# Optimization experiments

Measured on AMD Instinct MI355X. Metric: run time of the kernel, lower is better.

The kernel has to match this reference:

```python
import jax, jax.numpy as jnp
import numpy as np

FEAT_STRIDE = 8
SCALES = (4.0, 8.0, 16.0)
RATIOS = (0.5, 1.0, 2.0)
A = len(SCALES) * len(RATIOS)          # 9 anchors per location
PRE_NMS = 2048
POST_NMS = 300
NMS_THRESH = 0.7


def _gen_base_anchors():
    # cube anchors at scale*stride, ratio applied to depth; boxes (x1,y1,z1,x2,y2,z2)
    base = float(FEAT_STRIDE)
    ctr = (base - 1.0) / 2.0
    boxes = []
    for r in RATIOS:
        for s in SCALES:
            w = h = base * s
            d = base * s * r
            boxes.append([ctr - 0.5 * (w - 1), ctr - 0.5 * (h - 1), ctr - 0.5 * (d - 1),
                          ctr + 0.5 * (w - 1), ctr + 0.5 * (h - 1), ctr + 0.5 * (d - 1)])
    return jnp.asarray(boxes, jnp.float32)  # [A,6]


def _all_anchors(D, H, W):
    sz = jnp.arange(D, dtype=jnp.float32) * FEAT_STRIDE
    sy = jnp.arange(H, dtype=jnp.float32) * FEAT_STRIDE
    sx = jnp.arange(W, dtype=jnp.float32) * FEAT_STRIDE
    zz, yy, xx = jnp.meshgrid(sz, sy, sx, indexing='ij')  # order (d,h,w) matches score layout
    shifts = jnp.stack([xx, yy, zz, xx, yy, zz], -1).reshape(-1, 6)  # [K,6]
    return (shifts[:, None, :] + _gen_base_anchors()[None]).reshape(-1, 6)  # [K*A,6]


def _apply_deltas(anchors, deltas):
    w = anchors[:, 3] - anchors[:, 0] + 1.0
    h = anchors[:, 4] - anchors[:, 1] + 1.0
    d = anchors[:, 5] - anchors[:, 2] + 1.0
    cx = anchors[:, 0] + 0.5 * w
    cy = anchors[:, 1] + 0.5 * h
    cz = anchors[:, 2] + 0.5 * d
    dx, dy, dz, dw, dh, dd = [deltas[:, i] for i in range(6)]
    pcx = dx * w + cx; pcy = dy * h + cy; pcz = dz * d + cz
    pw = jnp.exp(dw) * w; ph = jnp.exp(dh) * h; pd = jnp.exp(dd) * d
    return jnp.stack([pcx - 0.5 * pw, pcy - 0.5 * ph, pcz - 0.5 * pd,
                      pcx + 0.5 * pw, pcy + 0.5 * ph, pcz + 0.5 * pd], -1)


def _clip_boxes(boxes, iminfo):  # iminfo = [D_im, H_im, W_im]
    lo = jnp.zeros((6,), boxes.dtype)
    hi = jnp.stack([iminfo[2], iminfo[1], iminfo[0], iminfo[2], iminfo[1], iminfo[0]]) - 1.0
    return jnp.clip(boxes, lo[None, :], hi[None, :])


def _pairwise_iou3d(b):  # b: [N,6]
    lo = jnp.maximum(b[:, None, :3], b[None, :, :3])          # [N,N,3]
    hi = jnp.minimum(b[:, None, 3:], b[None, :, 3:])
    inter = jnp.prod(jnp.clip(hi - lo + 1.0, 0.0), axis=-1)   # [N,N]
    vol = jnp.prod(b[:, 3:] - b[:, :3] + 1.0, axis=-1)        # [N]
    return inter / (vol[:, None] + vol[None, :] - inter)


def _nms_keep(iou):
    N = iou.shape[0]
    idx = jnp.arange(N)
    def body(i, keep):
        sup = (iou[i] > NMS_THRESH) & keep[i] & (idx > i)
        return keep & ~sup
    return jax.lax.fori_loop(0, N, body, jnp.ones((N,), bool))


def _propose_one(scores, deltas, anchors, iminfo):
    boxes = _clip_boxes(_apply_deltas(anchors, deltas), iminfo)  # [KA,6]
    _, order = jax.lax.top_k(scores, PRE_NMS)
    b = boxes[order]                                             # [PRE,6], score-sorted desc
    keep = _nms_keep(_pairwise_iou3d(b))
    key = jnp.where(keep, jnp.arange(PRE_NMS), PRE_NMS)
    sel = jnp.argsort(key)[:POST_NMS]                            # first POST_NMS kept, in score order
    valid = (key[sel] < PRE_NMS).astype(b.dtype)
    return b[sel] * valid[:, None]                               # zero-padded rows if < POST_NMS kept


def _forward(base_feat, im_info, W_conv, b_conv, W_cls, b_cls, W_bbox, b_bbox):
    B, C, D, H, W = base_feat.shape
    x = jax.lax.conv_general_dilated(
        base_feat, W_conv, (1, 1, 1), ((1, 1), (1, 1), (1, 1)),
        dimension_numbers=('NCDHW', 'OIDHW', 'NCDHW'))
    x = jax.nn.relu(x + b_conv[None, :, None, None, None])       # [B,512,D,H,W]
    cls = jnp.einsum('bcdhw,oc->bodhw', x, W_cls) + b_cls[None, :, None, None, None]
    prob = jax.nn.softmax(cls.reshape(B, 2, A, D, H, W), axis=1)  # reshape(x,2) + softmax(dim=1)
    fg = prob[:, 1]                                               # [B,A,D,H,W]
    scores = jnp.transpose(fg, (0, 2, 3, 4, 1)).reshape(B, -1)    # [B, K*A], order (d,h,w,a)
    bb = jnp.einsum('bcdhw,oc->bodhw', x, W_bbox) + b_bbox[None, :, None, None, None]
    deltas = jnp.transpose(bb.reshape(B, A, 6, D, H, W), (0, 3, 4, 5, 1, 2)).reshape(B, -1, 6)
    anchors = _all_anchors(D, H, W)
    rois6 = jax.vmap(lambda s, d, im: _propose_one(s, d, anchors, im))(scores, deltas, im_info)
    bidx = jnp.broadcast_to(jnp.arange(B, dtype=rois6.dtype)[:, None, None], (B, POST_NMS, 1))
    return jnp.concatenate([bidx, rois6], -1)                     # [B, POST_NMS, 7]


def setup_inputs() -> dict:
    key = jax.random.key(0)
    ks = jax.random.split(key, 4)
    B, din, D, H, W = 2, 128, 8, 32, 32
    base_feat = jax.random.normal(ks[0], (B, din, D, H, W), jnp.float32)
    im_info = jnp.asarray([[64.0, 256.0, 256.0]] * B, jnp.float32)  # (D_im, H_im, W_im)
    gt_boxes = jnp.zeros((B, 20, 7), jnp.float32)
    num_boxes = jnp.zeros((B,), jnp.int64)
    W_conv = jax.random.normal(ks[1], (512, din, 3, 3, 3), jnp.float32) * 0.02
    b_conv = jnp.zeros((512,), jnp.float32)
    W_cls = jax.random.normal(ks[2], (2 * A, 512), jnp.float32) * 0.01
    b_cls = jnp.zeros((2 * A,), jnp.float32)
    W_bbox = jax.random.normal(ks[3], (6 * A, 512), jnp.float32) * 0.01
    b_bbox = jnp.zeros((6 * A,), jnp.float32)
    return {"base_feat": base_feat, "im_info": im_info, "gt_boxes": gt_boxes,
            "num_boxes": num_boxes, "W_conv": W_conv, "b_conv": b_conv,
            "W_cls": W_cls, "b_cls": b_cls, "W_bbox": W_bbox, "b_bbox": b_bbox}


def reference(base_feat, im_info, gt_boxes, num_boxes, W_conv, b_conv, W_cls, b_cls, W_bbox, b_bbox):
    # Eval-mode RPN forward: losses are 0 in the original; gt_boxes/num_boxes unused.
    rois = _forward(base_feat, im_info, W_conv, b_conv, W_cls, b_cls, W_bbox, b_bbox)
    return rois
```

## Files before the change

kernel.cpp:

```cpp
#include <hip/hip_runtime.h>
#include <stdint.h>

#define BATCH 2
#define CIN 128
#define COUT 512
#define DD 8
#define PSPAT 8192
#define NA 9
#define NANCH 73728
#define PRE 2048
#define POST 300
#define CAP 4096
#define NMS_TH 0.7f

typedef unsigned short u16;
typedef _Float16 f16x8 __attribute__((ext_vector_type(8)));
typedef float f32x16 __attribute__((ext_vector_type(16)));
typedef unsigned int uint32x4 __attribute__((ext_vector_type(4)));

constexpr size_t OFF_WT   = 0;
constexpr size_t OFF_WHT  = 7077888;
constexpr size_t OFF_X    = 7241728;
constexpr size_t OFF_SC   = 40796160;
constexpr size_t OFF_BX   = 41385984;
constexpr size_t OFF_SB   = 44957696;
constexpr size_t OFF_MK   = 45056000;
constexpr size_t OFF_HIST = 16;
constexpr size_t OFF_CAND = 524304;
constexpr size_t OFF_XH   = 46104576;
constexpr size_t OFF_XL   = 50298880;
constexpr size_t WS_NEED_FAST = 54493184;

#define NT_WT   (27 * 128 * 512)
#define NT_WHT  (512 * 80)
__global__ void k_wtrans(const float* __restrict__ Wc, u16* __restrict__ Wg,
                         const float* __restrict__ Wcls, const float* __restrict__ Wbb,
                         float* __restrict__ Wht) {
    int e = blockIdx.x * blockDim.x + threadIdx.x;
    if (e < NT_WT) {
        const int k    = e & 63;
        const int n    = (e >> 6) & 127;
        const int half = (e >> 13) & 1;
        const int rest = e >> 14;
        const int co = (rest / 27) * 128 + n;
        const int ci = half * 64 + k;
        const int tp = rest % 27;
        const float v = Wc[(co * 128 + ci) * 27 + tp] * 1024.f;
        const _Float16 h = (_Float16)v;
        const _Float16 l = (_Float16)(v - (float)h);
        char* rb = (char*)Wg + (((size_t)(rest * 2 + half)) << 15) + n * 256;
        const int hcol = (k >> 3) ^ (n & 15);
        const int lcol = ((k >> 3) | 8) ^ (n & 15);
        const int kb = (k & 7) << 1;
        *(u16*)(rb + (hcol << 4) + kb) = __builtin_bit_cast(unsigned short, h);
        *(u16*)(rb + (lcol << 4) + kb) = __builtin_bit_cast(unsigned short, l);
        return;
    }
    e -= NT_WT;
    if (e >= NT_WHT) return;
    int q = e % 80;
    int c = e / 80;
    int og = q / 10, k = q % 10;
    int o = og * 9 + k;
    float v = 0.f;
    if (k < 9) v = (o < 18) ? Wcls[o * 512 + c] : Wbb[(o - 18) * 512 + c];
    Wht[e] = v;
}

__global__ __launch_bounds__(256) void k_split(const float* __restrict__ in,
                                               u16* __restrict__ xh, u16* __restrict__ xl) {
    __shared__ float t[128][33];
    const int blk = blockIdx.x;
    const int b = blk >> 8, d = (blk >> 5) & 7, h = blk & 31;
    const int tid = threadIdx.x;
    const float* src = in + ((size_t)b << 20) + d * 1024 + h * 32;
    #pragma unroll
    for (int i = 0; i < 16; ++i) {
        const int e = tid + i * 256;
        const int ci = e >> 5, w = e & 31;
        t[ci][w] = src[(size_t)ci * 8192 + w];
    }
    __syncthreads();
    const size_t ob = (size_t)((b * 8 + d) * 32 + h) * 4096;
    #pragma unroll
    for (int i = 0; i < 2; ++i) {
        const int e = tid + i * 256;
        const int oct = e >> 5, w = e & 31;
        unsigned sh0, sh1, sh2, sh3, sl0, sl1, sl2, sl3;
        #define SPL2(C, SH, SL) { \
            const float va_ = t[oct * 8 + 2*(C)][w] * 1024.f; \
            const float vb_ = t[oct * 8 + 2*(C)+1][w] * 1024.f; \
            const _Float16 ha_ = (_Float16)va_, hb_ = (_Float16)vb_; \
            const _Float16 la_ = (_Float16)(va_ - (float)ha_); \
            const _Float16 lb_ = (_Float16)(vb_ - (float)hb_); \
            SH = (unsigned)__builtin_bit_cast(unsigned short, ha_) | \
                 ((unsigned)__builtin_bit_cast(unsigned short, hb_) << 16); \
            SL = (unsigned)__builtin_bit_cast(unsigned short, la_) | \
                 ((unsigned)__builtin_bit_cast(unsigned short, lb_) << 16); }
        SPL2(0, sh0, sl0) SPL2(1, sh1, sl1) SPL2(2, sh2, sl2) SPL2(3, sh3, sl3)
        #undef SPL2
        uint32x4 vh = {sh0, sh1, sh2, sh3};
        uint32x4 vl = {sl0, sl1, sl2, sl3};
        *(uint32x4*)(xh + ob + (size_t)e * 8) = vh;
        *(uint32x4*)(xl + ob + (size_t)e * 8) = vl;
    }
}

#define MFMA(A, B, C) __builtin_amdgcn_mfma_f32_32x32x16_f16((A), (B), (C), 0, 0, 0)
#define Z16 {0.f,0.f,0.f,0.f,0.f,0.f,0.f,0.f,0.f,0.f,0.f,0.f,0.f,0.f,0.f,0.f}

#define WISSUE(S, BUF) { \
    const int tap_ = t0 + ((S) >> 1); \
    const char* gw_ = WgB + (((size_t)((nt * 27 + tap_) * 2 + ((S) & 1))) << 15) \
                    + (wv << 13) + ln16; \
    char* lb_ = smem + ((BUF) << 15) + (wv << 13); \
    _Pragma("unroll") \
    for (int j_ = 0; j_ < 8; ++j_) \
        __builtin_amdgcn_global_load_lds( \
            (const __attribute__((address_space(1))) void*)(gw_ + (j_ << 10)), \
            (__attribute__((address_space(3))) void*)(lb_ + (j_ << 10)), 16, 0, 0); }

#define KKSTEP(KK, BH0, BL0, BH1, BL1) { \
    const int ch_ = ((((KK) << 1) + cq) ^ rsw) << 4; \
    const int cl_ = (((((KK) << 1) + cq) | 8) ^ rsw) << 4; \
    const char* r0_ = wb_ + (rm0 << 8); \
    const char* r1_ = wb_ + (rm1 << 8); \
    const f16x8 wh0 = *(const f16x8*)(r0_ + ch_); \
    const f16x8 wl0 = *(const f16x8*)(r0_ + cl_); \
    const f16x8 wh1 = *(const f16x8*)(r1_ + ch_); \
    const f16x8 wl1 = *(const f16x8*)(r1_ + cl_); \
    acc00 = MFMA(wh0, BH0, acc00); \
    acc01 = MFMA(wh0, BH1, acc01); \
    acc10 = MFMA(wh1, BH0, acc10); \
    acc11 = MFMA(wh1, BH1, acc11); \
    acc00 = MFMA(wh0, BL0, acc00); \
    acc01 = MFMA(wh0, BL1, acc01); \
    acc10 = MFMA(wh1, BL0, acc10); \
    acc11 = MFMA(wh1, BL1, acc11); \
    acc00 = MFMA(wl0, BH0, acc00); \
    acc01 = MFMA(wl0, BH1, acc01); \
    acc10 = MFMA(wl1, BH0, acc10); \
    acc11 = MFMA(wl1, BH1, acc11); }

#define EPI(ACC, MI, NI) { \
    const int coB_ = co0 + (wm << 6) + ((MI) << 5) + hl4; \
    const int pt_  = p0 + (wn << 6) + ((NI) << 5) + l31; \
    _Pragma("unroll") \
    for (int g_ = 0; g_ < 4; ++g_) { \
        _Pragma("unroll") \
        for (int q_ = 0; q_ < 4; ++q_) { \
            const int co_ = coB_ + (g_ << 3) + q_; \
            const float v_ = ACC[g_ * 4 + q_] * 9.5367431640625e-07f + bconv[co_]; \
            x[((size_t)((b << 9) + co_) << 13) + pt_] = fmaxf(v_, 0.f); \
        } } }

#define FLD(N, KK, BH, BL) { \
    const int h2_ = hb_ + (N); \
    const bool ok_ = okw_ && ((unsigned)h2_ < 32u); \
    const size_t ix_ = sbase_ + ((size_t)(h2_ & 31) << 12); \
    const f16x8 vh_ = *(const f16x8*)(xh + ix_ + ((KK) << 9)); \
    const f16x8 vl_ = *(const f16x8*)(xl + ix_ + ((KK) << 9)); \
    BH = ok_ ? vh_ : fz8; \
    BL = ok_ ? vl_ : fz8; }

#define ALOADF(S, P) { \
    const int tap_ = t0 + ((S) >> 1); \
    const int kd_ = tap_ / 9, kh_ = (tap_ / 3) % 3, kw_ = tap_ % 3; \
    const int id_ = d0 + kd_ - 1; \
    const int w2_ = l31 + kw_ - 1; \
    const bool okw_ = (unsigned)w2_ < 32u; \
    const int hb_ = h0 + (wn << 1) + kh_ - 1; \
    const int oc0_ = (((S) & 1) << 3) + cq; \
    const size_t sbase_ = (((size_t)((b << 3) + id_)) << 17) + (oc0_ << 8) + ((w2_ & 31) << 3); \
    FLD(0, 0, P##h00, P##l00) FLD(0, 1, P##h01, P##l01) \
    FLD(0, 2, P##h02, P##l02) FLD(0, 3, P##h03, P##l03) \
    FLD(1, 0, P##h10, P##l10) FLD(1, 1, P##h11, P##l11) \
    FLD(1, 2, P##h12, P##l12) FLD(1, 3, P##h13, P##l13) }

#define COMPUTEF(BUF, P) { \
    const char* wb_ = smem + ((BUF) << 15); \
    KKSTEP(0, P##h00, P##l00, P##h10, P##l10) \
    KKSTEP(1, P##h01, P##l01, P##h11, P##l11) \
    KKSTEP(2, P##h02, P##l02, P##h12, P##l12) \
    KKSTEP(3, P##h03, P##l03, P##h13, P##l13) }

#define VMCNT24 asm volatile("s_waitcnt vmcnt(24)" ::: "memory");
#define VMCNT16 asm volatile("s_waitcnt vmcnt(16)" ::: "memory");
#define VMCNT0  asm volatile("s_waitcnt vmcnt(0)"  ::: "memory");
#define SBAR    __builtin_amdgcn_s_barrier();
#define SCHED0  __builtin_amdgcn_sched_barrier(0);

__global__ __launch_bounds__(256, 2) void k_conv_f(const u16* __restrict__ xh,
                                                   const u16* __restrict__ xl,
                                                   const u16* __restrict__ Wg,
                                                   const float* __restrict__ bconv,
                                                   float* __restrict__ x) {
    __shared__ __align__(16) char smem[65536];
    const int tid  = threadIdx.x;
    const int bx   = blockIdx.x;
    const int nt   = blockIdx.y;
    const int b    = blockIdx.z;
    const int p0   = bx << 7;
    const int d0   = bx >> 3;
    const int h0   = (bx & 7) << 2;
    const int co0  = nt << 7;

    const int lane = tid & 63;
    const int wv   = tid >> 6;
    const int wm   = wv & 1;
    const int wn   = wv >> 1;
    const int l31  = lane & 31;
    const int cq   = lane >> 5;
    const int hl4  = cq << 2;
    const int rsw  = l31 & 15;
    const int rm0  = (wm << 6) + l31;
    const int rm1  = rm0 + 32;
    const int ln16 = lane << 4;

    const int t0   = (d0 == 0) ? 9 : 0;
    const int nTap = 27 - (((d0 == 0) || (d0 == 7)) ? 9 : 0);
    const int NS   = nTap * 2;

    const char* WgB = (const char*)Wg;
    const f16x8 fz8 = {(_Float16)0.f, (_Float16)0.f, (_Float16)0.f, (_Float16)0.f,
                       (_Float16)0.f, (_Float16)0.f, (_Float16)0.f, (_Float16)0.f};

    f16x8 Ah00, Al00, Ah01, Al01, Ah02, Al02, Ah03, Al03,
          Ah10, Al10, Ah11, Al11, Ah12, Al12, Ah13, Al13;
    f16x8 Bh00, Bl00, Bh01, Bl01, Bh02, Bl02, Bh03, Bl03,
          Bh10, Bl10, Bh11, Bl11, Bh12, Bl12, Bh13, Bl13;
    f32x16 acc00 = Z16, acc01 = Z16, acc10 = Z16, acc11 = Z16;

    WISSUE(0, 0)
    SCHED0
    ALOADF(0, A)
    VMCNT16
    SBAR

    for (int s = 0; s < NS; s += 2) {
        WISSUE(s + 1, 1)
        SCHED0
        ALOADF(s + 1, B)
        VMCNT24
        SCHED0
        COMPUTEF(0, A)
        VMCNT16
        SBAR
        if (s + 2 < NS) {
            WISSUE(s + 2, 0)
            SCHED0
            ALOADF(s + 2, A)
            VMCNT24
        } else {
            VMCNT0
        }
        SCHED0
        COMPUTEF(1, B)
        if (s + 2 < NS) {
            VMCNT16
            SBAR
        }
    }

    EPI(acc00, 0, 0)
    EPI(acc01, 0, 1)
    EPI(acc10, 1, 0)
    EPI(acc11, 1, 1)
}

#define PK2(YA, YB, UH, UL) { \
    const float sa_ = (YA) * 1024.f, sb_ = (YB) * 1024.f; \
    const _Float16 ha_ = (_Float16)sa_, hb_ = (_Float16)sb_; \
    const _Float16 la_ = (_Float16)(sa_ - (float)ha_); \
    const _Float16 lb_ = (_Float16)(sb_ - (float)hb_); \
    UH = (unsigned)__builtin_bit_cast(unsigned short, ha_) | \
         ((unsigned)__builtin_bit_cast(unsigned short, hb_) << 16); \
    UL = (unsigned)__builtin_bit_cast(unsigned short, la_) | \
         ((unsigned)__builtin_bit_cast(unsigned short, lb_) << 16); }

#define BLDI(N, KK) { \
    const int h2_ = hb_ + (N); \
    const bool ok_ = okw_ && ((unsigned)h2_ < 32u); \
    const float* ap_ = in + (((size_t)(cb0_ + ((KK) << 4))) << 13) + spo_ + (h2_ << 5); \
    y[N][KK][0] = ok_ ? ap_[0]     : 0.f; \
    y[N][KK][1] = ok_ ? ap_[8192]  : 0.f; \
    y[N][KK][2] = ok_ ? ap_[16384] : 0.f; \
    y[N][KK][3] = ok_ ? ap_[24576] : 0.f; \
    y[N][KK][4] = ok_ ? ap_[32768] : 0.f; \
    y[N][KK][5] = ok_ ? ap_[40960] : 0.f; \
    y[N][KK][6] = ok_ ? ap_[49152] : 0.f; \
    y[N][KK][7] = ok_ ? ap_[57344] : 0.f; }

#define ALOADISS(S) { \
    const int tap_ = t0 + ((S) >> 1); \
    const int kd_ = tap_ / 9, kh_ = (tap_ / 3) % 3, kw_ = tap_ % 3; \
    const int id_ = d0 + kd_ - 1; \
    const int w2_ = l31 + kw_ - 1; \
    const bool okw_ = (unsigned)w2_ < 32u; \
    const int hb_ = h0 + (wn << 1) + kh_ - 1; \
    const int cb0_ = b * CIN + (((S) & 1) << 6) + (cq << 3); \
    const long long spo_ = ((long long)id_ << 10) + w2_; \
    BLDI(0, 0) BLDI(0, 1) BLDI(0, 2) BLDI(0, 3) \
    BLDI(1, 0) BLDI(1, 1) BLDI(1, 2) BLDI(1, 3) }

#define CVTFRAG(N, KK, BH, BL) { \
    unsigned uh0_, uh1_, uh2_, uh3_, ul0_, ul1_, ul2_, ul3_; \
    PK2(y[N][KK][0], y[N][KK][1], uh0_, ul0_) \
    PK2(y[N][KK][2], y[N][KK][3], uh1_, ul1_) \
    PK2(y[N][KK][4], y[N][KK][5], uh2_, ul2_) \
    PK2(y[N][KK][6], y[N][KK][7], uh3_, ul3_) \
    { uint32x4 th_ = {uh0_, uh1_, uh2_, uh3_}; BH = __builtin_bit_cast(f16x8, th_); } \
    { uint32x4 tl_ = {ul0_, ul1_, ul2_, ul3_}; BL = __builtin_bit_cast(f16x8, tl_); } }

#define CVTALL() { \
    CVTFRAG(0, 0, bh00, bl00) CVTFRAG(0, 1, bh01, bl01) \
    CVTFRAG(0, 2, bh02, bl02) CVTFRAG(0, 3, bh03, bl03) \
    CVTFRAG(1, 0, bh10, bl10) CVTFRAG(1, 1, bh11, bl11) \
    CVTFRAG(1, 2, bh12, bl12) CVTFRAG(1, 3, bh13, bl13) }

#define COMPUTE(BUF) { \
    const char* wb_ = smem + ((BUF) << 15); \
    KKSTEP(0, bh00, bl00, bh10, bl10) \
    KKSTEP(1, bh01, bl01, bh11, bl11) \
    KKSTEP(2, bh02, bl02, bh12, bl12) \
    KKSTEP(3, bh03, bl03, bh13, bl13) }

__global__ __launch_bounds__(256, 2) void k_conv(const float* __restrict__ in,
                                                 const u16* __restrict__ Wg,
                                                 const float* __restrict__ bconv,
                                                 float* __restrict__ x) {
    __shared__ __align__(16) char smem[65536];
    const int tid  = threadIdx.x;
    const int bx   = blockIdx.x;
    const int nt   = blockIdx.y;
    const int b    = blockIdx.z;
    const int p0   = bx << 7;
    const int d0   = bx >> 3;
    const int h0   = (bx & 7) << 2;
    const int co0  = nt << 7;

    const int lane = tid & 63;
    const int wv   = tid >> 6;
    const int wm   = wv & 1;
    const int wn   = wv >> 1;
    const int l31  = lane & 31;
    const int cq   = lane >> 5;
    const int hl4  = cq << 2;
    const int rsw  = l31 & 15;
    const int rm0  = (wm << 6) + l31;
    const int rm1  = rm0 + 32;
    const int ln16 = lane << 4;

    const int t0   = (d0 == 0) ? 9 : 0;
    const int nTap = 27 - (((d0 == 0) || (d0 == 7)) ? 9 : 0);
    const int NS   = nTap * 2;

    const char* WgB = (const char*)Wg;

    float y[2][4][8];
    f16x8 bh00, bh01, bh02, bh03, bh10, bh11, bh12, bh13;
    f16x8 bl00, bl01, bl02, bl03, bl10, bl11, bl12, bl13;
    f32x16 acc00 = Z16, acc01 = Z16, acc10 = Z16, acc11 = Z16;

    WISSUE(0, 0)
    ALOADISS(0)
    __syncthreads();

    for (int s = 0; s < NS; ++s) {
        if (s + 1 < NS) { WISSUE(s + 1, (s + 1) & 1) }
        CVTALL()
        __builtin_amdgcn_sched_barrier(0);
        if (s + 1 < NS) { ALOADISS(s + 1) }
        __builtin_amdgcn_sched_barrier(0);
        COMPUTE(s & 1)
        __syncthreads();
    }

    EPI(acc00, 0, 0)
    EPI(acc01, 0, 1)
    EPI(acc10, 1, 0)
    EPI(acc11, 1, 1)
}

__global__ __launch_bounds__(256) void k_heads(const float* __restrict__ x,
                                               const float* __restrict__ Wht,
                                               const float* __restrict__ bcls,
                                               const float* __restrict__ bbb,
                                               const float* __restrict__ iminfo,
                                               float* __restrict__ scores,
                                               float* __restrict__ boxes,
                                               unsigned int* __restrict__ hist) {
    __shared__ __align__(16) float smx[4096];
    __shared__ __align__(16) float Whs[2560];
    __shared__ __align__(16) float ex[10240];
    const int tid = threadIdx.x;
    const int p0  = blockIdx.x * 128;
    const int b   = blockIdx.y;
    const int pl  = tid & 31;
    const int og  = tid >> 5;

    float acc[4][9] = {};

    for (int cc = 0; cc < 512; cc += 32) {
        __syncthreads();
        #pragma unroll
        for (int i = 0; i < 4; ++i) {
            int e4 = tid + i * 256;
            int ch = e4 >> 5;
            int pt4 = (e4 & 31) * 4;
            *(float4*)&smx[ch * 128 + pt4] =
                *(const float4*)&x[((size_t)(b * COUT + cc + ch) << 13) + p0 + pt4];
        }
        #pragma unroll
        for (int i = 0; i < 10; ++i) {
            int e = tid + i * 256;
            Whs[e] = Wht[cc * 80 + e];
        }
        __syncthreads();
        for (int kk = 0; kk < 32; ++kk) {
            float4 a4 = *(const float4*)&smx[kk * 128 + pl * 4];
            const float* wp = &Whs[kk * 80 + og * 10];
            float2 w0 = *(const float2*)(wp);
            float2 w1 = *(const float2*)(wp + 2);
            float2 w2 = *(const float2*)(wp + 4);
            float2 w3 = *(const float2*)(wp + 6);
            float  w8 = wp[8];
            float wv[9] = {w0.x, w0.y, w1.x, w1.y, w2.x, w2.y, w3.x, w3.y, w8};
            #pragma unroll
            for (int k = 0; k < 9; ++k) {
                float wk = wv[k];
                acc[0][k] += a4.x * wk;
                acc[1][k] += a4.y * wk;
                acc[2][k] += a4.z * wk;
                acc[3][k] += a4.w * wk;
            }
        }
    }

    __syncthreads();
    #pragma unroll
    for (int pi = 0; pi < 4; ++pi)
        #pragma unroll
        for (int k = 0; k < 9; ++k)
            ex[(pl * 4 + pi) * 80 + og * 10 + k] = acc[pi][k];
    __syncthreads();

    if (tid < 128) {
        const int p = p0 + tid;
        float v[72];
        #pragma unroll
        for (int og2 = 0; og2 < 8; ++og2)
            #pragma unroll
            for (int k = 0; k < 9; ++k)
                v[og2 * 9 + k] = ex[tid * 80 + og2 * 10 + k];

        const float im0 = iminfo[b * 3 + 0], im1 = iminfo[b * 3 + 1], im2 = iminfo[b * 3 + 2];
        const float hix = im2 - 1.f, hiy = im1 - 1.f, hiz = im0 - 1.f;
        const int d = p >> 10, h = (p >> 5) & 31, w = p & 31;
        const float sx = w * 8.f, sy = h * 8.f, sz = d * 8.f;

        #pragma unroll 1
        for (int a = 0; a < 9; ++a) {
            float c0 = v[a] + bcls[a];
            float c1 = v[9 + a] + bcls[9 + a];
            float m  = fmaxf(c0, c1);
            float e0 = expf(c0 - m), e1 = expf(c1 - m);
            float sc = e1 / (e0 + e1);
            scores[b * NANCH + p * 9 + a] = sc;
            atomicAdd(&hist[b * 65536 + (__float_as_uint(sc) >> 16)], 1u);

            float aw = (float)(32 << (a % 3));
            float ad = aw * 0.5f * (float)(1 << (a / 3));
            float ax1 = sx + 3.5f - 0.5f * (aw - 1.f);
            float ax2 = sx + 3.5f + 0.5f * (aw - 1.f);
            float ay1 = sy + 3.5f - 0.5f * (aw - 1.f);
            float ay2 = sy + 3.5f + 0.5f * (aw - 1.f);
            float az1 = sz + 3.5f - 0.5f * (ad - 1.f);
            float az2 = sz + 3.5f + 0.5f * (ad - 1.f);
            float ww_ = ax2 - ax1 + 1.f, hh_ = ay2 - ay1 + 1.f, dd_ = az2 - az1 + 1.f;
            float cx = ax1 + 0.5f * ww_, cy = ay1 + 0.5f * hh_, cz = az1 + 0.5f * dd_;

            const float* dv = &v[18 + a * 6];
            float dx = dv[0] + bbb[a * 6 + 0];
            float dy = dv[1] + bbb[a * 6 + 1];
            float dz = dv[2] + bbb[a * 6 + 2];
            float dw = dv[3] + bbb[a * 6 + 3];
            float dh = dv[4] + bbb[a * 6 + 4];
            float dd2 = dv[5] + bbb[a * 6 + 5];
            float pcx = dx * ww_ + cx, pcy = dy * hh_ + cy, pcz = dz * dd_ + cz;
            float pw = expf(dw) * ww_, ph = expf(dh) * hh_, pd = expf(dd2) * dd_;
            float x1 = fminf(fmaxf(pcx - 0.5f * pw, 0.f), hix);
            float y1 = fminf(fmaxf(pcy - 0.5f * ph, 0.f), hiy);
            float z1 = fminf(fmaxf(pcz - 0.5f * pd, 0.f), hiz);
            float x2 = fminf(fmaxf(pcx + 0.5f * pw, 0.f), hix);
            float y2 = fminf(fmaxf(pcy + 0.5f * ph, 0.f), hiy);
            float z2 = fminf(fmaxf(pcz + 0.5f * pd, 0.f), hiz);
            float* bp = &boxes[(size_t)(b * NANCH + p * 9 + a) * 6];
            bp[0] = x1; bp[1] = y1; bp[2] = z1; bp[3] = x2; bp[4] = y2; bp[5] = z2;
        }
    }
}

__global__ __launch_bounds__(1024) void k_cutcompact(const float* __restrict__ scores,
                                                     const unsigned int* __restrict__ hist,
                                                     unsigned long long* __restrict__ cand) {
    __shared__ unsigned int cs[1024], scan[1024];
    __shared__ unsigned int sh_cut, sh_pos;
    const int b = blockIdx.x, tid = threadIdx.x;
    const unsigned int* h = hist + b * 65536;
    unsigned int s = 0;
    for (int i = 0; i < 64; ++i) s += h[tid * 64 + i];
    cs[tid] = s; scan[tid] = s;
    if (tid == 0) sh_pos = 0;
    __syncthreads();
    for (int d = 1; d < 1024; d <<= 1) {
        unsigned int v = scan[tid];
        unsigned int add = (tid + d < 1024) ? scan[tid + d] : 0u;
        __syncthreads();
        scan[tid] = v + add;
        __syncthreads();
    }
    unsigned int above = (tid + 1 < 1024) ? scan[tid + 1] : 0u;
    if (above < PRE && above + cs[tid] >= PRE) {
        unsigned int cum = above;
        for (int x = tid * 64 + 63; x >= tid * 64; --x) {
            cum += h[x];
            if (cum >= PRE) { sh_cut = (unsigned int)x; break; }
        }
    }
    __syncthreads();
    const unsigned int cut = sh_cut;
    const float* sc = scores + b * NANCH;
    for (int i = tid; i < NANCH; i += 1024) {
        unsigned int u = __float_as_uint(sc[i]);
        if ((u >> 16) >= cut) {
            unsigned int pos = atomicAdd(&sh_pos, 1u);
            if (pos < CAP) cand[b * CAP + pos] = ((unsigned long long)(~u) << 32) | (unsigned)i;
        }
    }
    __syncthreads();
    const unsigned int cnt = (sh_pos < CAP) ? sh_pos : CAP;
    for (int i = (int)cnt + tid; i < CAP; i += 1024)
        cand[b * CAP + i] = ~0ull;
}

__global__ __launch_bounds__(1024) void k_sort2(const unsigned long long* __restrict__ cand,
                                                const float* __restrict__ boxes,
                                                float* __restrict__ sboxes) {
    __shared__ unsigned long long sk[CAP];
    const int b = blockIdx.x, tid = threadIdx.x;
    for (int i = tid; i < CAP; i += 1024) sk[i] = cand[b * CAP + i];
    __syncthreads();
    for (int k = 2; k <= CAP; k <<= 1) {
        for (int j = k >> 1; j > 0; j >>= 1) {
            #pragma unroll 1
            for (int i = tid; i < CAP; i += 1024) {
                int ixj = i ^ j;
                if (ixj > i) {
                    unsigned long long va = sk[i], vb = sk[ixj];
                    bool up = ((i & k) == 0);
                    if ((va > vb) == up) { sk[i] = vb; sk[ixj] = va; }
                }
            }
            __syncthreads();
        }
    }
    for (int r = tid; r < PRE; r += 1024) {
        unsigned int n = (unsigned int)(sk[r] & 0xFFFFFFFFull);
        const float* src = &boxes[(size_t)(b * NANCH + (int)n) * 6];
        float* dst = &sboxes[(size_t)(b * PRE + r) * 6];
        #pragma unroll
        for (int c = 0; c < 6; ++c) dst[c] = src[c];
    }
}

__global__ __launch_bounds__(256) void k_mask(const float* __restrict__ sboxes,
                                              unsigned long long* __restrict__ mask) {
    if (blockIdx.y < blockIdx.x) return;
    __shared__ float rb[64 * 6], cb[64 * 6];
    const int i0 = blockIdx.x * 64, j0 = blockIdx.y * 64, b = blockIdx.z;
    const int tid = threadIdx.x;
    for (int e = tid; e < 384; e += 256) {
        rb[e] = sboxes[(size_t)(b * PRE + i0) * 6 + e];
        cb[e] = sboxes[(size_t)(b * PRE + j0) * 6 + e];
    }
    __syncthreads();
    const int wave = tid >> 6, lane = tid & 63;
    const float bx1 = cb[lane * 6 + 0], by1 = cb[lane * 6 + 1], bz1 = cb[lane * 6 + 2];
    const float bx2 = cb[lane * 6 + 3], by2 = cb[lane * 6 + 4], bz2 = cb[lane * 6 + 5];
    const float vb = (bx2 - bx1 + 1.f) * (by2 - by1 + 1.f) * (bz2 - bz1 + 1.f);
    const int j = j0 + lane;
    for (int rr = 0; rr < 16; ++rr) {
        const int il = wave * 16 + rr;
        const int i = i0 + il;
        float ax1 = rb[il * 6 + 0], ay1 = rb[il * 6 + 1], az1 = rb[il * 6 + 2];
        float ax2 = rb[il * 6 + 3], ay2 = rb[il * 6 + 4], az2 = rb[il * 6 + 5];
        float va = (ax2 - ax1 + 1.f) * (ay2 - ay1 + 1.f) * (az2 - az1 + 1.f);
        float ix = fmaxf(fminf(ax2, bx2) - fmaxf(ax1, bx1) + 1.f, 0.f);
        float iy = fmaxf(fminf(ay2, by2) - fmaxf(ay1, by1) + 1.f, 0.f);
        float iz = fmaxf(fminf(az2, bz2) - fmaxf(az1, bz1) + 1.f, 0.f);
        float inter = ix * iy * iz;
        float iou = inter / (va + vb - inter);
        bool bit = (j > i) && (iou > NMS_TH);
        unsigned long long word = __ballot(bit);
        if (lane == 0) mask[(size_t)(b * PRE + i) * 32 + (j0 >> 6)] = word;
    }
}

__global__ __launch_bounds__(64) void k_nms(const unsigned long long* __restrict__ mask,
                                            const float* __restrict__ sboxes,
                                            float* __restrict__ out) {
    const int b = blockIdx.x, lane = threadIdx.x;
    __shared__ int sel[POST];
    unsigned long long keep = ~0ull;
    const int lw = lane & 31;
    const unsigned long long* mrow = mask + (size_t)b * PRE * 32 + lw;
    unsigned long long b0 = mrow[0 * 32], b1 = mrow[1 * 32], b2 = mrow[2 * 32], b3 = mrow[3 * 32];
    unsigned long long b4 = mrow[4 * 32], b5 = mrow[5 * 32], b6 = mrow[6 * 32], b7 = mrow[7 * 32];
    int kcount = 0;

#define NMS_STEP(J, BUF)                                                        \
    {                                                                           \
        int i = i0 + (J);                                                       \
        unsigned long long cur = (lw >= (i >> 6)) ? BUF : 0ull;                 \
        int nr = i0 + 8 + (J);                                                  \
        BUF = (nr < PRE) ? mrow[(size_t)nr * 32] : 0ull;                        \
        unsigned long long kw = __shfl(keep, i >> 6);                           \
        if ((kw >> (i & 63)) & 1ull) {                                          \
            if (lane < 32) keep &= ~cur;                                        \
            if (lane == 0 && kcount < POST) sel[kcount] = i;                    \
            ++kcount;                                                           \
            if (kcount >= POST) goto nms_done;                                  \
        }                                                                       \
    }

    for (int i0 = 0; i0 < PRE; i0 += 8) {
        NMS_STEP(0, b0) NMS_STEP(1, b1) NMS_STEP(2, b2) NMS_STEP(3, b3)
        NMS_STEP(4, b4) NMS_STEP(5, b5) NMS_STEP(6, b6) NMS_STEP(7, b7)
    }
nms_done:
    __syncthreads();
    const int kc = kcount;
    for (int r = lane; r < POST; r += 64) {
        float* op = &out[(size_t)(b * POST + r) * 7];
        op[0] = (float)b;
        if (r < kc) {
            const float* sb = &sboxes[(size_t)(b * PRE + sel[r]) * 6];
            #pragma unroll
            for (int c = 0; c < 6; ++c) op[1 + c] = sb[c];
        } else {
            #pragma unroll
            for (int c = 0; c < 6; ++c) op[1 + c] = 0.f;
        }
    }
#undef NMS_STEP
}

extern "C" void kernel_launch(void* const* d_in, const int* in_sizes, int n_in,
                              void* d_out, int out_size, void* d_ws, size_t ws_size,
                              hipStream_t stream) {
    const float* base_feat = (const float*)d_in[0];
    const float* im_info   = (const float*)d_in[1];
    const float* W_conv    = (const float*)d_in[4];
    const float* b_conv    = (const float*)d_in[5];
    const float* W_cls     = (const float*)d_in[6];
    const float* b_cls     = (const float*)d_in[7];
    const float* W_bbox    = (const float*)d_in[8];
    const float* b_bbox    = (const float*)d_in[9];

    char* ws = (char*)d_ws;
    u16* Wg        = (u16*)(ws + OFF_WT);
    float* Wht     = (float*)(ws + OFF_WHT);
    float* x       = (float*)(ws + OFF_X);
    float* scores  = (float*)(ws + OFF_SC);
    float* boxes   = (float*)(ws + OFF_BX);
    float* sboxes  = (float*)(ws + OFF_SB);
    unsigned long long* mask = (unsigned long long*)(ws + OFF_MK);
    unsigned int* hist = (unsigned int*)(ws + OFF_HIST);
    unsigned long long* cand = (unsigned long long*)(ws + OFF_CAND);
    u16* xh        = (u16*)(ws + OFF_XH);
    u16* xl        = (u16*)(ws + OFF_XL);

    const int NTRANS = NT_WT + NT_WHT;
    k_wtrans<<<(NTRANS + 255) / 256, 256, 0, stream>>>(W_conv, Wg, W_cls, W_bbox, Wht);
    if (ws_size >= WS_NEED_FAST) {
        k_split<<<512, 256, 0, stream>>>(base_feat, xh, xl);
        k_conv_f<<<dim3(64, 4, 2), 256, 0, stream>>>(xh, xl, Wg, b_conv, x);
    } else {
        k_conv<<<dim3(64, 4, 2), 256, 0, stream>>>(base_feat, Wg, b_conv, x);
    }
    hipMemsetAsync(hist, 0, BATCH * 65536 * sizeof(unsigned int), stream);
    k_heads<<<dim3(64, 2), 256, 0, stream>>>(x, Wht, b_cls, b_bbox, im_info, scores, boxes, hist);
    k_cutcompact<<<BATCH, 1024, 0, stream>>>(scores, hist, cand);
    k_sort2<<<BATCH, 1024, 0, stream>>>(cand, boxes, sboxes);
    k_mask<<<dim3(32, 32, 2), 256, 0, stream>>>(sboxes, mask);
    k_nms<<<BATCH, 64, 0, stream>>>(mask, sboxes, (float*)d_out);
}
```

Before: 557.1 us.

## Halve conv output-channel tile to 64, use 2-wave blocks and raise MFMA priority

The fused conv kernel now handles 64 output channels per block instead of 128. It uses 128 threads (2 waves split along the spatial dimension only) and 32KB of shared memory, and launches twice as many blocks along the channel axis. The weight pre-transform layout is changed to match the 64-channel tiles. s_setprio is raised around the MFMA compute section. The unused fallback non-split conv path is removed. This aims to improve occupancy and the number of blocks available to fill the GPU, but each block has less weight reuse and the input activations are loaded twice as often.

```diff
diff --git a/kernel.cpp b/kernel.cpp
--- a/kernel.cpp
+++ b/kernel.cpp
@@ -29,7 +29,6 @@
 constexpr size_t OFF_CAND = 524304;
 constexpr size_t OFF_XH   = 46104576;
 constexpr size_t OFF_XL   = 50298880;
-constexpr size_t WS_NEED_FAST = 54493184;
 
 #define NT_WT   (27 * 128 * 512)
 #define NT_WHT  (512 * 80)
@@ -39,16 +38,16 @@
     int e = blockIdx.x * blockDim.x + threadIdx.x;
     if (e < NT_WT) {
         const int k    = e & 63;
-        const int n    = (e >> 6) & 127;
-        const int half = (e >> 13) & 1;
-        const int rest = e >> 14;
-        const int co = (rest / 27) * 128 + n;
+        const int n    = (e >> 6) & 63;
+        const int half = (e >> 12) & 1;
+        const int rest = e >> 13;
+        const int co = (rest / 27) * 64 + n;
         const int ci = half * 64 + k;
         const int tp = rest % 27;
         const float v = Wc[(co * 128 + ci) * 27 + tp] * 1024.f;
         const _Float16 h = (_Float16)v;
         const _Float16 l = (_Float16)(v - (float)h);
-        char* rb = (char*)Wg + (((size_t)(rest * 2 + half)) << 15) + n * 256;
+        char* rb = (char*)Wg + (((size_t)(rest * 2 + half)) << 14) + n * 256;
         const int hcol = (k >> 3) ^ (n & 15);
         const int lcol = ((k >> 3) | 8) ^ (n & 15);
         const int kb = (k & 7) << 1;
@@ -111,9 +110,9 @@
 
 #define WISSUE(S, BUF) { \
     const int tap_ = t0 + ((S) >> 1); \
-    const char* gw_ = WgB + (((size_t)((nt * 27 + tap_) * 2 + ((S) & 1))) << 15) \
+    const char* gw_ = WgB + (((size_t)((nt * 27 + tap_) * 2 + ((S) & 1))) << 14) \
                     + (wv << 13) + ln16; \
-    char* lb_ = smem + ((BUF) << 15) + (wv << 13); \
+    char* lb_ = smem + ((BUF) << 14) + (wv << 13); \
     _Pragma("unroll") \
     for (int j_ = 0; j_ < 8; ++j_) \
         __builtin_amdgcn_global_load_lds( \
@@ -143,7 +142,7 @@
     acc11 = MFMA(wl1, BH1, acc11); }
 
 #define EPI(ACC, MI, NI) { \
-    const int coB_ = co0 + (wm << 6) + ((MI) << 5) + hl4; \
+    const int coB_ = co0 + ((MI) << 5) + hl4; \
     const int pt_  = p0 + (wn << 6) + ((NI) << 5) + l31; \
     _Pragma("unroll") \
     for (int g_ = 0; g_ < 4; ++g_) { \
@@ -178,11 +177,13 @@
     FLD(1, 2, P##h12, P##l12) FLD(1, 3, P##h13, P##l13) }
 
 #define COMPUTEF(BUF, P) { \
-    const char* wb_ = smem + ((BUF) << 15); \
+    const char* wb_ = smem + ((BUF) << 14); \
+    __builtin_amdgcn_s_setprio(1); \
     KKSTEP(0, P##h00, P##l00, P##h10, P##l10) \
     KKSTEP(1, P##h01, P##l01, P##h11, P##l11) \
     KKSTEP(2, P##h02, P##l02, P##h12, P##l12) \
-    KKSTEP(3, P##h03, P##l03, P##h13, P##l13) }
+    KKSTEP(3, P##h03, P##l03, P##h13, P##l13) \
+    __builtin_amdgcn_s_setprio(0); }
 
 #define VMCNT24 asm volatile("s_waitcnt vmcnt(24)" ::: "memory");
 #define VMCNT16 asm volatile("s_waitcnt vmcnt(16)" ::: "memory");
@@ -190,12 +191,12 @@
 #define SBAR    __builtin_amdgcn_s_barrier();
 #define SCHED0  __builtin_amdgcn_sched_barrier(0);
 
-__global__ __launch_bounds__(256, 2) void k_conv_f(const u16* __restrict__ xh,
+__global__ __launch_bounds__(128, 2) void k_conv_f(const u16* __restrict__ xh,
                                                    const u16* __restrict__ xl,
                                                    const u16* __restrict__ Wg,
                                                    const float* __restrict__ bconv,
                                                    float* __restrict__ x) {
-    __shared__ __align__(16) char smem[65536];
+    __shared__ __align__(16) char smem[32768];
     const int tid  = threadIdx.x;
     const int bx   = blockIdx.x;
     const int nt   = blockIdx.y;
@@ -203,18 +204,17 @@
     const int p0   = bx << 7;
     const int d0   = bx >> 3;
     const int h0   = (bx & 7) << 2;
-    const int co0  = nt << 7;
+    const int co0  = nt << 6;
 
     const int lane = tid & 63;
     const int wv   = tid >> 6;
-    const int wm   = wv & 1;
-    const int wn   = wv >> 1;
+    const int wn   = wv;
     const int l31  = lane & 31;
     const int cq   = lane >> 5;
     const int hl4  = cq << 2;
     const int rsw  = l31 & 15;
-    const int rm0  = (wm << 6) + l31;
-    const int rm1  = rm0 + 32;
+    const int rm0  = l31;
+    const int rm1  = l31 + 32;
     const int ln16 = lane << 4;
 
     const int t0   = (d0 == 0) ? 9 : 0;
@@ -260,120 +260,6 @@
             VMCNT16
             SBAR
         }
-    }
-
-    EPI(acc00, 0, 0)
-    EPI(acc01, 0, 1)
-    EPI(acc10, 1, 0)
-    EPI(acc11, 1, 1)
-}
-
-#define PK2(YA, YB, UH, UL) { \
-    const float sa_ = (YA) * 1024.f, sb_ = (YB) * 1024.f; \
-    const _Float16 ha_ = (_Float16)sa_, hb_ = (_Float16)sb_; \
-    const _Float16 la_ = (_Float16)(sa_ - (float)ha_); \
-    const _Float16 lb_ = (_Float16)(sb_ - (float)hb_); \
-    UH = (unsigned)__builtin_bit_cast(unsigned short, ha_) | \
-         ((unsigned)__builtin_bit_cast(unsigned short, hb_) << 16); \
-    UL = (unsigned)__builtin_bit_cast(unsigned short, la_) | \
-         ((unsigned)__builtin_bit_cast(unsigned short, lb_) << 16); }
-
-#define BLDI(N, KK) { \
-    const int h2_ = hb_ + (N); \
-    const bool ok_ = okw_ && ((unsigned)h2_ < 32u); \
-    const float* ap_ = in + (((size_t)(cb0_ + ((KK) << 4))) << 13) + spo_ + (h2_ << 5); \
-    y[N][KK][0] = ok_ ? ap_[0]     : 0.f; \
-    y[N][KK][1] = ok_ ? ap_[8192]  : 0.f; \
-    y[N][KK][2] = ok_ ? ap_[16384] : 0.f; \
-    y[N][KK][3] = ok_ ? ap_[24576] : 0.f; \
-    y[N][KK][4] = ok_ ? ap_[32768] : 0.f; \
-    y[N][KK][5] = ok_ ? ap_[40960] : 0.f; \
-    y[N][KK][6] = ok_ ? ap_[49152] : 0.f; \
-    y[N][KK][7] = ok_ ? ap_[57344] : 0.f; }
-
-#define ALOADISS(S) { \
-    const int tap_ = t0 + ((S) >> 1); \
-    const int kd_ = tap_ / 9, kh_ = (tap_ / 3) % 3, kw_ = tap_ % 3; \
-    const int id_ = d0 + kd_ - 1; \
-    const int w2_ = l31 + kw_ - 1; \
-    const bool okw_ = (unsigned)w2_ < 32u; \
-    const int hb_ = h0 + (wn << 1) + kh_ - 1; \
-    const int cb0_ = b * CIN + (((S) & 1) << 6) + (cq << 3); \
-    const long long spo_ = ((long long)id_ << 10) + w2_; \
-    BLDI(0, 0) BLDI(0, 1) BLDI(0, 2) BLDI(0, 3) \
-    BLDI(1, 0) BLDI(1, 1) BLDI(1, 2) BLDI(1, 3) }
-
-#define CVTFRAG(N, KK, BH, BL) { \
-    unsigned uh0_, uh1_, uh2_, uh3_, ul0_, ul1_, ul2_, ul3_; \
-    PK2(y[N][KK][0], y[N][KK][1], uh0_, ul0_) \
-    PK2(y[N][KK][2], y[N][KK][3], uh1_, ul1_) \
-    PK2(y[N][KK][4], y[N][KK][5], uh2_, ul2_) \
-    PK2(y[N][KK][6], y[N][KK][7], uh3_, ul3_) \
-    { uint32x4 th_ = {uh0_, uh1_, uh2_, uh3_}; BH = __builtin_bit_cast(f16x8, th_); } \
-    { uint32x4 tl_ = {ul0_, ul1_, ul2_, ul3_}; BL = __builtin_bit_cast(f16x8, tl_); } }
-
-#define CVTALL() { \
-    CVTFRAG(0, 0, bh00, bl00) CVTFRAG(0, 1, bh01, bl01) \
-    CVTFRAG(0, 2, bh02, bl02) CVTFRAG(0, 3, bh03, bl03) \
-    CVTFRAG(1, 0, bh10, bl10) CVTFRAG(1, 1, bh11, bl11) \
-    CVTFRAG(1, 2, bh12, bl12) CVTFRAG(1, 3, bh13, bl13) }
-
-#define COMPUTE(BUF) { \
-    const char* wb_ = smem + ((BUF) << 15); \
-    KKSTEP(0, bh00, bl00, bh10, bl10) \
-    KKSTEP(1, bh01, bl01, bh11, bl11) \
-    KKSTEP(2, bh02, bl02, bh12, bl12) \
-    KKSTEP(3, bh03, bl03, bh13, bl13) }
-
-__global__ __launch_bounds__(256, 2) void k_conv(const float* __restrict__ in,
-                                                 const u16* __restrict__ Wg,
-                                                 const float* __restrict__ bconv,
-                                                 float* __restrict__ x) {
-    __shared__ __align__(16) char smem[65536];
-    const int tid  = threadIdx.x;
-    const int bx   = blockIdx.x;
-    const int nt   = blockIdx.y;
-    const int b    = blockIdx.z;
-    const int p0   = bx << 7;
-    const int d0   = bx >> 3;
-    const int h0   = (bx & 7) << 2;
-    const int co0  = nt << 7;
-
-    const int lane = tid & 63;
-    const int wv   = tid >> 6;
-    const int wm   = wv & 1;
-    const int wn   = wv >> 1;
-    const int l31  = lane & 31;
-    const int cq   = lane >> 5;
-    const int hl4  = cq << 2;
-    const int rsw  = l31 & 15;
-    const int rm0  = (wm << 6) + l31;
-    const int rm1  = rm0 + 32;
-    const int ln16 = lane << 4;
-
-    const int t0   = (d0 == 0) ? 9 : 0;
-    const int nTap = 27 - (((d0 == 0) || (d0 == 7)) ? 9 : 0);
-    const int NS   = nTap * 2;
-
-    const char* WgB = (const char*)Wg;
-
-    float y[2][4][8];
-    f16x8 bh00, bh01, bh02, bh03, bh10, bh11, bh12, bh13;
-    f16x8 bl00, bl01, bl02, bl03, bl10, bl11, bl12, bl13;
-    f32x16 acc00 = Z16, acc01 = Z16, acc10 = Z16, acc11 = Z16;
-
-    WISSUE(0, 0)
-    ALOADISS(0)
-    __syncthreads();
-
-    for (int s = 0; s < NS; ++s) {
-        if (s + 1 < NS) { WISSUE(s + 1, (s + 1) & 1) }
-        CVTALL()
-        __builtin_amdgcn_sched_barrier(0);
-        if (s + 1 < NS) { ALOADISS(s + 1) }
-        __builtin_amdgcn_sched_barrier(0);
-        COMPUTE(s & 1)
-        __syncthreads();
     }
 
     EPI(acc00, 0, 0)
@@ -683,12 +569,8 @@
 
     const int NTRANS = NT_WT + NT_WHT;
     k_wtrans<<<(NTRANS + 255) / 256, 256, 0, stream>>>(W_conv, Wg, W_cls, W_bbox, Wht);
-    if (ws_size >= WS_NEED_FAST) {
-        k_split<<<512, 256, 0, stream>>>(base_feat, xh, xl);
-        k_conv_f<<<dim3(64, 4, 2), 256, 0, stream>>>(xh, xl, Wg, b_conv, x);
-    } else {
-        k_conv<<<dim3(64, 4, 2), 256, 0, stream>>>(base_feat, Wg, b_conv, x);
-    }
+    k_split<<<512, 256, 0, stream>>>(base_feat, xh, xl);
+    k_conv_f<<<dim3(64, 8, 2), 128, 0, stream>>>(xh, xl, Wg, b_conv, x);
     hipMemsetAsync(hist, 0, BATCH * 65536 * sizeof(unsigned int), stream);
     k_heads<<<dim3(64, 2), 256, 0, stream>>>(x, Wht, b_cls, b_bbox, im_info, scores, boxes, hist);
     k_cutcompact<<<BATCH, 1024, 0, stream>>>(scores, hist, cand);
```

Result: no change. 556.3 us (-0.1%).
